# Kernel optimization log

Hardware: AMD Instinct MI355X
Metric: run time of the kernel (lower is better)

## Reference

```python
import jax, jax.numpy as jnp
import numpy as np

D_RBF = 36
KMIN = 9
EPS_LN = 1e-5


def layer_norm(x, g, b):
    mu = x.mean(-1, keepdims=True)
    var = ((x - mu) ** 2).mean(-1, keepdims=True)
    return (x - mu) * jax.lax.rsqrt(var + EPS_LN) * g + b


def rbf(D):
    # radial basis expansion, 36 gaussians on [0, 20]
    mu = jnp.linspace(0.0, 20.0, D_RBF)
    sigma = 20.0 / D_RBF
    return jnp.exp(-(((D[..., None] - mu) / sigma) ** 2))


def cdist(a, b):
    d2 = jnp.sum((a[:, :, None, :] - b[:, None, :, :]) ** 2, -1)
    return jnp.sqrt(jnp.maximum(d2, 1e-12))


def setup_inputs() -> dict:
    key = jax.random.key(0)
    ks = iter(jax.random.split(key, 64))
    B, N, L = 1, 64, 512
    d_msa, d_pair, d_state = 64, 128, 16
    def nrm(shape, s=1.0):
        return jax.random.normal(next(ks), shape, jnp.float32) * s
    def lin(fin, fout):
        return nrm((fin, fout), 0.05), jnp.zeros((fout,), jnp.float32)
    def ln(d):
        return jnp.ones((d,), jnp.float32), jnp.zeros((d,), jnp.float32)
    inp = {}
    inp['msa'] = nrm((B, N, L, d_msa))
    inp['pair'] = nrm((B, L, L, d_pair))
    inp['xyz'] = nrm((B, L, 3, 3), 8.0)  # spread coords so kNN is meaningful
    inp['state'] = nrm((B, L, d_state))
    inp['seq1hot'] = jax.nn.one_hot(jax.random.randint(next(ks), (B, L), 0, 21), 21, dtype=jnp.float32)
    inp['idx'] = jnp.broadcast_to(jnp.arange(L, dtype=jnp.int32)[None], (B, L))
    inp['top_k'] = 64
    inp['g_msa'], inp['b_msa'] = ln(d_msa)
    inp['g_pair'], inp['b_pair'] = ln(d_pair)
    inp['g_state'], inp['b_state'] = ln(d_state)
    inp['Wq'], inp['bq'] = lin(d_msa, d_msa)
    inp['Wk'], inp['bk'] = lin(d_msa, d_msa)
    inp['Wx'], inp['bx'] = lin(d_msa + 21 + d_state, 32)
    inp['We1'], inp['be1'] = lin(d_pair, 32)
    inp['We2'], inp['be2'] = lin(32 + D_RBF + 1, 32)
    inp['g_node'], inp['b_node'] = ln(32)
    inp['g_e1'], inp['b_e1'] = ln(32)
    inp['g_e2'], inp['b_e2'] = ln(32)
    # SE3-style equivariant MP layer params
    inp['Wm1'], inp['bm1'] = lin(32 + 32 + 32 + 1, 64)
    inp['Wm2'], inp['bm2'] = lin(64, 32)
    inp['Wc'], inp['bc'] = lin(32, 8)      # 2 out vec channels x (1 coef for d + 3 for v_src)
    inp['Wh'], inp['bh'] = lin(64, 16)     # l0 out
    inp['Wv'] = nrm((2, 3), 0.05)          # l1 channel mixing
    return inp


def reference(msa, pair, xyz, state, seq1hot, idx, top_k,
              g_msa, b_msa, g_pair, b_pair, g_state, b_state,
              Wq, bq, Wk, bk, Wx, bx, We1, be1, We2, be2,
              g_node, b_node, g_e1, b_e1, g_e2, b_e2,
              Wm1, bm1, Wm2, bm2, Wc, bc, Wh, bh, Wv):
    eps = 1e-5
    B, N, L, K = msa.shape
    msa = layer_norm(msa, g_msa, b_msa)
    pair = layer_norm(pair, g_pair, b_pair)
    state = layer_norm(state, g_state, b_state)

    # SequenceWeight (1 head): first-seq query attends over N sequences per position
    q = (msa[:, 0] @ Wq + bq) / jnp.sqrt(jnp.float32(K))       # (B,L,K)
    k = jnp.einsum('bnlk,kd->bnld', msa, Wk) + bk              # (B,N,L,K)
    attn = jax.nn.softmax(jnp.einsum('blk,bnlk->bnl', q, k), axis=1)
    msa1 = jnp.einsum('bnl,bnlk->blk', attn, msa)              # (B,L,K)

    node = jnp.concatenate([msa1, seq1hot, state], -1)
    node = layer_norm(node @ Wx + bx, g_node, b_node)          # (B,L,32)
    edge = layer_norm(pair @ We1 + be1, g_e1, b_e1)            # (B,L,L,32)

    sep = idx[:, None, :] - idx[:, :, None]                    # (B,L,L)
    neighbor = jnp.where(jnp.abs(sep) <= 1, sep, 0).astype(node.dtype)[..., None]
    ca = xyz[:, :, 1]                                          # (B,L,3)
    rbf_feat = rbf(cdist(ca, ca))
    edge = jnp.concatenate([edge, rbf_feat, neighbor], -1)
    edge = layer_norm(edge @ We2 + be2, g_e2, b_e2)            # (B,L,L,32)

    # kNN + sequence-separation graph, as a dense boolean mask (edge i->j)
    eye = jnp.eye(L)[None]
    D = cdist(ca, ca) + eye * 999.9
    sep_a = jnp.abs(sep).astype(jnp.float32) + eye * 999.9
    kk = min(int(top_k), L)
    _, E_idx = jax.lax.top_k(-jax.lax.stop_gradient(D), kk)    # (B,L,kk) nearest j per i
    bi = jnp.arange(B)[:, None, None]
    ii = jnp.arange(L)[None, :, None]
    mask = jnp.zeros((B, L, L), bool).at[bi, ii, E_idx].set(True)
    mask = jnp.logical_or(mask, sep_a < KMIN)
    maskf = mask.astype(node.dtype)

    v = xyz - ca[:, :, None, :]                                # l1 feats (B,L,3,3)
    dvec = jax.lax.stop_gradient(ca[:, None, :, :] - ca[:, :, None, :])  # d[b,i,j]=ca_j-ca_i
    dist = jnp.linalg.norm(dvec, axis=-1, keepdims=True)       # (B,L,L,1)

    # invariant scalar messages (avoid materializing concat: split Wm1)
    hid = (node @ Wm1[:32])[:, :, None, :] + (node @ Wm1[32:64])[:, None, :, :] \
        + edge @ Wm1[64:96] + dist * Wm1[96] + bm1
    hid = jax.nn.relu(hid)                                     # (B,L,L,64)
    m = jax.nn.relu(hid @ Wm2 + bm2)                           # (B,L,L,32)
    coef = (m @ Wc + bc).reshape(B, L, L, 2, 4)
    # equivariant vector messages: coef0 * d_ij + sum_c coef_c * v_i[c]
    vmsg = coef[..., 0:1] * dvec[:, :, :, None, :] \
         + jnp.einsum('bijoc,bicv->bijov', coef[..., 1:], v)   # (B,L,L,2,3)
    agg_m = jnp.einsum('bij,bijk->bjk', maskf, m)              # aggregate at target j
    agg_v = jnp.einsum('bij,bijov->bjov', maskf, vmsg)

    state_out = jnp.concatenate([node, agg_m], -1) @ Wh + bh   # shift['0'] -> (B,L,16)
    off = agg_v + jnp.einsum('oc,blcv->blov', Wv, v)           # shift['1'] -> (B,L,2,3)

    # Rodrigues rotation + translation update
    T = off[:, :, 0]
    R = off[:, :, 1]
    ang = jnp.linalg.norm(R, axis=-1, keepdims=True)           # (B,L,1)
    Rv = (R / (ang + eps))[:, :, None, :]                      # (B,L,1,3)
    Rdv = jnp.sum(Rv * v, -1, keepdims=True)                   # (B,L,3,1)
    Rxv = jnp.cross(jnp.broadcast_to(Rv, v.shape), v)
    vperp = v - Rv * Rdv
    upar = Rv * Rdv
    c = jnp.cos(ang)[:, :, None, :]
    s = jnp.sin(ang)[:, :, None, :]
    v_new = vperp * c + Rxv * s + upar
    xyz_new = v_new + (ca + T)[:, :, None, :]
    return xyz_new, state_out
```

## Files before the change

### kernel.cpp

```cpp
#include <hip/hip_runtime.h>
#include <hip/hip_bf16.h>

typedef __attribute__((ext_vector_type(8))) short short8v;
typedef __attribute__((ext_vector_type(4))) float f32x4;

__device__ __forceinline__ unsigned short f2bu(float a){
  union { __hip_bfloat16 b; unsigned short u; } cv;
  cv.b = __float2bfloat16(a);
  return cv.u;
}
__device__ __forceinline__ void sp2(float a, unsigned short &h, unsigned short &l){
  h = f2bu(a);
  l = f2bu(a - __uint_as_float(((unsigned)h)<<16));
}
__device__ __forceinline__ float wred64(float v){
  #pragma unroll
  for(int o=32;o;o>>=1) v += __shfl_xor(v,o,64);
  return v;
}
__device__ __forceinline__ float wred32(float v){
  #pragma unroll
  for(int o=16;o;o>>=1) v += __shfl_xor(v,o,64);
  return v;
}
__device__ __forceinline__ float wmax64(float v){
  #pragma unroll
  for(int o=32;o;o>>=1) v = fmaxf(v,__shfl_xor(v,o,64));
  return v;
}

__global__ void __launch_bounds__(256) k_ctx(
  const float* __restrict__ msa, const float* __restrict__ g_msa, const float* __restrict__ b_msa,
  const float* __restrict__ Wq, const float* __restrict__ bq,
  const float* __restrict__ Wk, const float* __restrict__ bk,
  const float* __restrict__ seq1hot, const float* __restrict__ state,
  const float* __restrict__ g_state, const float* __restrict__ b_state,
  const float* __restrict__ Wx, const float* __restrict__ bx,
  const float* __restrict__ g_node, const float* __restrict__ b_node,
  const float* __restrict__ Wm1,
  float* __restrict__ node, float* __restrict__ nodeA, float* __restrict__ nodeB,
  const float* __restrict__ ca, const int* __restrict__ idx,
  const int* __restrict__ topk_ptr, unsigned char* __restrict__ maskT)
{
  int l = blockIdx.x, tid = threadIdx.x;
  int wave = tid>>6, lane = tid&63;
  __shared__ float ms[64][64];
  __shared__ float qs[64];
  __shared__ float logit[64];
  __shared__ float part[4][64];
  __shared__ float ins[101];
  __shared__ float nd[32];

  {
    int nn = tid>>2, qd = tid&3;
    const float* mrow = msa + ((size_t)nn*512 + (size_t)l)*64 + qd*16;
    f32x4 a[4];
    #pragma unroll
    for(int t=0;t<4;t++) a[t] = *(const f32x4*)(mrow + t*4);
    float s=0.f, ss=0.f;
    #pragma unroll
    for(int t=0;t<4;t++)
      #pragma unroll
      for(int e=0;e<4;e++){ float v=a[t][e]; s+=v; ss+=v*v; }
    s  += __shfl_xor(s,1,64);  s  += __shfl_xor(s,2,64);
    ss += __shfl_xor(ss,1,64); ss += __shfl_xor(ss,2,64);
    float mu = s*(1.f/64.f);
    float rstd = rsqrtf(ss*(1.f/64.f) - mu*mu + 1e-5f);
    #pragma unroll
    for(int t=0;t<4;t++){
      f32x4 g4 = *(const f32x4*)(g_msa + qd*16 + t*4);
      f32x4 b4 = *(const f32x4*)(b_msa + qd*16 + t*4);
      f32x4 o4;
      #pragma unroll
      for(int e=0;e<4;e++) o4[e] = (a[t][e]-mu)*rstd*g4[e] + b4[e];
      *(f32x4*)&ms[nn][qd*16 + t*4] = o4;
    }
  }
  __syncthreads();
  if(wave==0){
    float acc = bq[lane];
    for(int k=0;k<64;k++) acc += ms[0][k]*Wq[k*64+lane];
    qs[lane] = acc*0.125f;
  }
  __syncthreads();
  float qd2 = qs[lane];
  for(int it=0; it<16; ++it){
    int nn = it*4 + wave;
    float acc = bk[lane];
    for(int k2=0;k2<64;k2++) acc += ms[nn][k2]*Wk[k2*64+lane];
    float p = wred64(qd2*acc);
    if(lane==0) logit[nn] = p;
  }
  __syncthreads();
  float v  = logit[lane];
  float mx = wmax64(v);
  float e  = expf(v-mx);
  float sd = wred64(e);
  float a  = e/sd;
  float pm = 0.f;
  for(int it=0; it<16; ++it){
    int nn = it*4 + wave;
    pm += __shfl(a,nn,64)*ms[nn][lane];
  }
  part[wave][lane] = pm;
  __syncthreads();
  if(wave==0){
    ins[lane] = part[0][lane]+part[1][lane]+part[2][lane]+part[3][lane];
    if(lane<21) ins[64+lane] = seq1hot[l*21+lane];
    float sv = (lane<16)? state[l*16+lane] : 0.f;
    float mu = sv;
    #pragma unroll
    for(int o=8;o;o>>=1) mu += __shfl_xor(mu,o,64);
    mu *= (1.f/16.f);
    float dv = sv-mu;
    float var = dv*dv;
    #pragma unroll
    for(int o=8;o;o>>=1) var += __shfl_xor(var,o,64);
    var *= (1.f/16.f);
    if(lane<16) ins[85+lane] = dv*rsqrtf(var+1e-5f)*g_state[lane]+b_state[lane];

    int d = lane & 31;
    float np_ = 0.f;
    if(lane<32){
      np_ = bx[d];
      for(int c=0;c<101;c++) np_ += ins[c]*Wx[c*32+d];
    }
    float mu2 = wred32(np_)*(1.f/32.f);
    float d2  = np_-mu2;
    float v2  = wred32(d2*d2)*(1.f/32.f);
    float nv  = d2*rsqrtf(v2+1e-5f);
    if(lane<32){
      nv = nv*g_node[d]+b_node[d];
      node[l*32+d] = nv;
      nd[d] = nv;
    }
    float a2=0.f, b2=0.f;
    for(int c=0;c<32;c++){
      float x = nd[c];
      a2 += x*Wm1[c*64+lane];
      b2 += x*Wm1[(32+c)*64+lane];
    }
    nodeA[l*64+lane] = a2;
    nodeB[l*64+lane] = b2;
  } else if(wave==1){
    int i = l;
    float cx = ca[i*3], cy = ca[i*3+1], cz = ca[i*3+2];
    int idxi = idx[i];
    unsigned long long key[8];
    #pragma unroll
    for(int t=0;t<8;t++){
      int jj = t*64 + lane;
      float dx = cx-ca[jj*3], dy = cy-ca[jj*3+1], dz = cz-ca[jj*3+2];
      float dd = sqrtf(fmaxf(dx*dx+dy*dy+dz*dz, 1e-12f));
      if(jj==i) dd += 999.9f;
      key[t] = (((unsigned long long)__float_as_uint(dd))<<32) | (unsigned)jj;
      int sep = abs(idx[jj]-idxi);
      maskT[jj*512+i] = (jj!=i && sep<9) ? 1 : 0;
    }
    int kk = *topk_ptr; if(kk>512) kk = 512;
    for(int t=0;t<kk;t++){
      unsigned long long m = key[0];
      #pragma unroll
      for(int u=1;u<8;u++) m = (key[u]<m)? key[u] : m;
      #pragma unroll
      for(int o=32;o;o>>=1){
        unsigned long long o2 = __shfl_xor(m,o,64);
        m = (o2<m)? o2 : m;
      }
      int jc = (int)(m & 0xffffffffu);
      if(lane==0) maskT[jc*512+i] = 1;
      #pragma unroll
      for(int u=0;u<8;u++) if(key[u]==m) key[u] = ~0ull;
    }
  }
}

__global__ void k_fold(const float* __restrict__ We1, const float* __restrict__ be1,
                       const float* __restrict__ g_pair, const float* __restrict__ b_pair,
                       const float* __restrict__ We2, const float* __restrict__ be2,
                       const float* __restrict__ g_e1, const float* __restrict__ b_e1,
                       const float* __restrict__ Wm1, const float* __restrict__ bm1,
                       const float* __restrict__ g_e2, const float* __restrict__ b_e2,
                       const float* __restrict__ Wm2, const float* __restrict__ Wc,
                       const float* __restrict__ xyz,
                       unsigned short* __restrict__ wbuf, float* __restrict__ bbuf,
                       float* __restrict__ ca, float* __restrict__ vv){
  int fidx = blockIdx.x;
  int tid  = threadIdx.x;
  if(fidx < 46){
    int t = fidx*512 + tid;
    int lane = tid>>3, e = tid&7;
    int f = (fidx<23)? fidx : fidx-23;
    int krow = (lane>>4)*8 + e;
    int n = lane&15;
    float val = 0.f;
    if(f<8){
      int kt=f>>1, nt=f&1; int c=kt*32+krow, d=nt*16+n;
      val = g_pair[c]*We1[c*32+d];
    } else if(f<14){
      int f2=f-8; int kt=f2>>1, nt=f2&1; int c=kt*32+krow, d=nt*16+n;
      if(c<32)      val = g_e1[c]*We2[c*32+d];
      else if(c<69) val = We2[c*32+d];
      else          val = 0.f;
    } else if(f<18){
      int nt=f-14; int c=krow, h=nt*16+n;
      val = g_e2[c]*Wm1[(64+c)*64+h];
    } else if(f<22){
      int f2=f-18; int kt=f2>>1, nt=f2&1; int c=kt*32+krow, d=nt*16+n;
      val = Wm2[c*32+d];
    } else {
      int c=krow;
      val = (n<8)? Wc[c*8+n] : 0.f;
    }
    unsigned short h = f2bu(val);
    if(fidx<23) wbuf[t] = h;
    else {
      float fh = __uint_as_float(((unsigned)h)<<16);
      wbuf[t] = f2bu(val - fh);
    }
  } else if(fidx == 46){
    if(tid<32){
      float s = be1[tid];
      for(int c=0;c<128;c++) s += b_pair[c]*We1[c*32+tid];
      bbuf[tid]=s;
    } else if(tid<64){
      int d=tid-32; float s=be2[d];
      for(int c=0;c<32;c++) s += b_e1[c]*We2[c*32+d];
      bbuf[tid]=s;
    } else if(tid<128){
      int h=tid-64; float s=bm1[h];
      for(int c=0;c<32;c++) s += b_e2[c]*Wm1[(64+c)*64+h];
      bbuf[tid]=s;
    }
  } else {
    int l = tid;
    float c0=xyz[l*9+3], c1=xyz[l*9+4], c2=xyz[l*9+5];
    ca[l*3+0]=c0; ca[l*3+1]=c1; ca[l*3+2]=c2;
    #pragma unroll
    for(int a2=0;a2<3;a2++){
      vv[l*9+a2*3+0]=xyz[l*9+a2*3+0]-c0;
      vv[l*9+a2*3+1]=xyz[l*9+a2*3+1]-c1;
      vv[l*9+a2*3+2]=xyz[l*9+a2*3+2]-c2;
    }
  }
}

__global__ void __launch_bounds__(256,2) k_pair_mfma(
  const float* __restrict__ pair, const unsigned short* __restrict__ wbuf,
  const float* __restrict__ bbuf, const float* __restrict__ Wm1,
  const float* __restrict__ bm2, const float* __restrict__ bc,
  const float* __restrict__ nodeA, const float* __restrict__ nodeB,
  const float* __restrict__ ca, const float* __restrict__ vv,
  const int* __restrict__ idx, const unsigned char* __restrict__ maskT,
  float* __restrict__ aggM, float* __restrict__ aggV)
{
  const int j = blockIdx.x, tid = threadIdx.x;
  const int wave = tid>>6, lane = tid&63;
  const int kg = lane>>4, n = lane&15;

  __shared__ __align__(16) unsigned short Yh[4][16*104];
  __shared__ __align__(16) unsigned short Yl[4][16*104];
  __shared__ __align__(16) unsigned short WloE[23*512];
  __shared__ float coefT[4][16*8];
  __shared__ float redM[4][32];
  __shared__ float redV[4][8];
  unsigned short* Yhw = Yh[wave];
  unsigned short* Ylw = Yl[wave];
  float* CT = coefT[wave];

  for(int t=tid; t<(23*512)/8; t+=256)
    ((uint4*)WloE)[t] = ((const uint4*)(wbuf + 23*512))[t];

  short8v wf[23];
  #pragma unroll
  for(int f=0; f<23; f++) wf[f] = *(const short8v*)(wbuf + f*512 + lane*8);

  const float be1f0 = bbuf[n],     be1f1 = bbuf[16+n];
  const float be2f0 = bbuf[32+n],  be2f1 = bbuf[48+n];
  float bm1n[4], wm1d[4];
  #pragma unroll
  for(int nt=0;nt<4;nt++){
    bm1n[nt] = bbuf[64+nt*16+n] + nodeB[j*64+nt*16+n];
    wm1d[nt] = Wm1[96*64+nt*16+n];
  }
  const float bm2r0 = bm2[n], bm2r1 = bm2[16+n];
  const float bcr = (n<8)? bc[n] : 0.f;
  const float cjx = ca[j*3], cjy = ca[j*3+1], cjz = ca[j*3+2];
  const int idxj = idx[j];

  __syncthreads();

  for(int t=lane; t<16*27; t+=64){ int r=t/27, c=69+t-r*27; Yhw[r*104+c]=0; Ylw[r*104+c]=0; }

  float accM0=0.f, accM1=0.f;
  float accV[6]={0.f,0.f,0.f,0.f,0.f,0.f};

  float x[4][8];
  {
    const float* prow0 = pair + (((size_t)(wave*16+n))*512 + (size_t)j)*128;
    #pragma unroll
    for(int kt=0;kt<4;kt++){
      *(f32x4*)&x[kt][0] = *(const f32x4*)(prow0 + kt*32 + kg*8);
      *(f32x4*)&x[kt][4] = *(const f32x4*)(prow0 + kt*32 + kg*8 + 4);
    }
  }

  for(int i0 = wave*16; i0 < 512; i0 += 64){
    float s=0.f, ss=0.f;
    #pragma unroll
    for(int kt=0;kt<4;kt++)
      #pragma unroll
      for(int e=0;e<8;e++){ float xv=x[kt][e]; s+=xv; ss+=xv*xv; }
    s  += __shfl_xor(s,16,64);  s  += __shfl_xor(s,32,64);
    ss += __shfl_xor(ss,16,64); ss += __shfl_xor(ss,32,64);
    float mu = s*(1.f/128.f);
    float rstd = rsqrtf(ss*(1.f/128.f) - mu*mu + 1e-5f);

    float xn[4][8];
    const bool hasNext = (i0+64 < 512);
    if(hasNext){
      const float* prown = pair + (((size_t)(i0+64+n))*512 + (size_t)j)*128;
      #pragma unroll
      for(int kt=0;kt<4;kt++){
        *(f32x4*)&xn[kt][0] = *(const f32x4*)(prown + kt*32 + kg*8);
        *(f32x4*)&xn[kt][4] = *(const f32x4*)(prown + kt*32 + kg*8 + 4);
      }
    }

    float na[4][4];
    #pragma unroll
    for(int q=0;q<4;q++)
      #pragma unroll
      for(int nt=0;nt<4;nt++)
        na[nt][q] = nodeA[(size_t)(i0+4*kg+q)*64 + nt*16+n];
    float mk[4];
    #pragma unroll
    for(int q=0;q<4;q++) mk[q] = (float)maskT[j*512 + i0+4*kg+q];
    float mkr = (float)maskT[j*512 + i0+n];
    const float* vr = vv + (i0+n)*9;
    float v00=vr[0], v01=vr[1], v02=vr[2];
    float v10=vr[3], v11=vr[4], v12=vr[5];
    float v20=vr[6], v21=vr[7], v22=vr[8];
    const float* cai = ca + (i0+n)*3;
    float cix=cai[0], ciy=cai[1], ciz=cai[2];
    int idxi_r = idx[i0+n];

    short8v xh[4], xl[4];
    #pragma unroll
    for(int kt=0;kt<4;kt++){
      #pragma unroll
      for(int e=0;e<8;e++){
        unsigned short h_, l_;
        sp2((x[kt][e]-mu)*rstd, h_, l_);
        xh[kt][e] = (short)h_;
        xl[kt][e] = (short)l_;
      }
    }

    f32x4 z0={0.f,0.f,0.f,0.f}, z1={0.f,0.f,0.f,0.f};
    #pragma unroll
    for(int kt=0;kt<4;kt++){
      short8v wlo0 = *(const short8v*)&WloE[(2*kt+0)*512 + lane*8];
      short8v wlo1 = *(const short8v*)&WloE[(2*kt+1)*512 + lane*8];
      z0 = __builtin_amdgcn_mfma_f32_16x16x32_bf16(xh[kt], wf[2*kt+0], z0, 0,0,0);
      z0 = __builtin_amdgcn_mfma_f32_16x16x32_bf16(xl[kt], wf[2*kt+0], z0, 0,0,0);
      z0 = __builtin_amdgcn_mfma_f32_16x16x32_bf16(xh[kt], wlo0,      z0, 0,0,0);
      z1 = __builtin_amdgcn_mfma_f32_16x16x32_bf16(xh[kt], wf[2*kt+1], z1, 0,0,0);
      z1 = __builtin_amdgcn_mfma_f32_16x16x32_bf16(xl[kt], wf[2*kt+1], z1, 0,0,0);
      z1 = __builtin_amdgcn_mfma_f32_16x16x32_bf16(xh[kt], wlo1,      z1, 0,0,0);
    }
    #pragma unroll
    for(int q=0;q<4;q++){
      float ev0 = z0[q] + be1f0;
      float ev1 = z1[q] + be1f1;
      float sq  = ev0+ev1;
      float sq2 = ev0*ev0+ev1*ev1;
      #pragma unroll
      for(int o=8;o;o>>=1){ sq+=__shfl_xor(sq,o,64); sq2+=__shfl_xor(sq2,o,64); }
      float m_ = sq*(1.f/32.f);
      float rs = rsqrtf(sq2*(1.f/32.f)-m_*m_+1e-5f);
      unsigned short h0,l0,h1,l1;
      sp2((ev0-m_)*rs, h0, l0);
      sp2((ev1-m_)*rs, h1, l1);
      int r = 4*kg+q;
      Yhw[r*104 + n]    = h0;
      Yhw[r*104 + 16+n] = h1;
      Ylw[r*104 + n]    = l0;
      Ylw[r*104 + 16+n] = l1;
    }

    float dxr = cjx-cix, dyr = cjy-ciy, dzr = cjz-ciz;
    float d2r = dxr*dxr+dyr*dyr+dzr*dzr;
    float dist_r = sqrtf(d2r);
    float drbf = sqrtf(fmaxf(d2r,1e-12f));
    #pragma unroll
    for(int sI=0;sI<9;sI++){
      int t = kg*9+sI;
      float u = (drbf - (float)t*(20.f/35.f))*1.8f;
      unsigned short h_, l_;
      sp2(__expf(-u*u), h_, l_);
      Yhw[n*104 + 32 + t] = h_;
      Ylw[n*104 + 32 + t] = l_;
    }
    if(kg==0){
      int sep = idxj - idxi_r;
      float nb = (sep>=-1 && sep<=1)?(float)sep:0.f;
      unsigned short h_, l_;
      sp2(nb, h_, l_);
      Yhw[n*104 + 68] = h_;
      Ylw[n*104 + 68] = l_;
    }

    short8v yh_[3], yl_[3];
    #pragma unroll
    for(int kt=0;kt<3;kt++){
      yh_[kt] = *(const short8v*)&Yhw[n*104 + kt*32 + kg*8];
      yl_[kt] = *(const short8v*)&Ylw[n*104 + kt*32 + kg*8];
    }
    f32x4 e2a0={0.f,0.f,0.f,0.f}, e2a1={0.f,0.f,0.f,0.f};
    #pragma unroll
    for(int kt=0;kt<3;kt++){
      short8v wlo0 = *(const short8v*)&WloE[(8+2*kt)*512 + lane*8];
      short8v wlo1 = *(const short8v*)&WloE[(9+2*kt)*512 + lane*8];
      e2a0 = __builtin_amdgcn_mfma_f32_16x16x32_bf16(yh_[kt], wf[8+2*kt], e2a0, 0,0,0);
      e2a0 = __builtin_amdgcn_mfma_f32_16x16x32_bf16(yl_[kt], wf[8+2*kt], e2a0, 0,0,0);
      e2a0 = __builtin_amdgcn_mfma_f32_16x16x32_bf16(yh_[kt], wlo0,      e2a0, 0,0,0);
      e2a1 = __builtin_amdgcn_mfma_f32_16x16x32_bf16(yh_[kt], wf[9+2*kt], e2a1, 0,0,0);
      e2a1 = __builtin_amdgcn_mfma_f32_16x16x32_bf16(yl_[kt], wf[9+2*kt], e2a1, 0,0,0);
      e2a1 = __builtin_amdgcn_mfma_f32_16x16x32_bf16(yh_[kt], wlo1,      e2a1, 0,0,0);
    }
    #pragma unroll
    for(int q=0;q<4;q++){
      float ev0 = e2a0[q]+be2f0;
      float ev1 = e2a1[q]+be2f1;
      float sq  = ev0+ev1;
      float sq2 = ev0*ev0+ev1*ev1;
      #pragma unroll
      for(int o=8;o;o>>=1){ sq+=__shfl_xor(sq,o,64); sq2+=__shfl_xor(sq2,o,64); }
      float m_ = sq*(1.f/32.f);
      float rs = rsqrtf(sq2*(1.f/32.f)-m_*m_+1e-5f);
      unsigned short h0,l0,h1,l1;
      sp2((ev0-m_)*rs, h0, l0);
      sp2((ev1-m_)*rs, h1, l1);
      int r = 4*kg+q;
      Yhw[r*104 + n]    = h0;
      Yhw[r*104 + 16+n] = h1;
      Ylw[r*104 + n]    = l0;
      Ylw[r*104 + 16+n] = l1;
    }

    short8v e2Ah = *(const short8v*)&Yhw[n*104 + kg*8];
    short8v e2Al = *(const short8v*)&Ylw[n*104 + kg*8];
    float dist_q[4];
    #pragma unroll
    for(int q=0;q<4;q++) dist_q[q] = __shfl(dist_r, 4*kg+q, 64);
    #pragma unroll
    for(int nt=0;nt<4;nt++){
      short8v wlo = *(const short8v*)&WloE[(14+nt)*512 + lane*8];
      f32x4 hacc = {0.f,0.f,0.f,0.f};
      hacc = __builtin_amdgcn_mfma_f32_16x16x32_bf16(e2Ah, wf[14+nt], hacc, 0,0,0);
      hacc = __builtin_amdgcn_mfma_f32_16x16x32_bf16(e2Al, wf[14+nt], hacc, 0,0,0);
      hacc = __builtin_amdgcn_mfma_f32_16x16x32_bf16(e2Ah, wlo,       hacc, 0,0,0);
      #pragma unroll
      for(int q=0;q<4;q++){
        float t_ = hacc[q] + bm1n[nt] + dist_q[q]*wm1d[nt] + na[nt][q];
        float hv = fmaxf(t_,0.f);
        unsigned short h_, l_;
        sp2(hv, h_, l_);
        Yhw[(4*kg+q)*104 + nt*16+n] = h_;
        Ylw[(4*kg+q)*104 + nt*16+n] = l_;
      }
    }

    short8v hAh[2], hAl[2];
    #pragma unroll
    for(int kt=0;kt<2;kt++){
      hAh[kt] = *(const short8v*)&Yhw[n*104 + kt*32 + kg*8];
      hAl[kt] = *(const short8v*)&Ylw[n*104 + kt*32 + kg*8];
    }
    f32x4 ma0={0.f,0.f,0.f,0.f}, ma1={0.f,0.f,0.f,0.f};
    #pragma unroll
    for(int kt=0;kt<2;kt++){
      short8v wlo0 = *(const short8v*)&WloE[(18+2*kt)*512 + lane*8];
      short8v wlo1 = *(const short8v*)&WloE[(19+2*kt)*512 + lane*8];
      ma0 = __builtin_amdgcn_mfma_f32_16x16x32_bf16(hAh[kt], wf[18+2*kt], ma0, 0,0,0);
      ma0 = __builtin_amdgcn_mfma_f32_16x16x32_bf16(hAl[kt], wf[18+2*kt], ma0, 0,0,0);
      ma0 = __builtin_amdgcn_mfma_f32_16x16x32_bf16(hAh[kt], wlo0,       ma0, 0,0,0);
      ma1 = __builtin_amdgcn_mfma_f32_16x16x32_bf16(hAh[kt], wf[19+2*kt], ma1, 0,0,0);
      ma1 = __builtin_amdgcn_mfma_f32_16x16x32_bf16(hAl[kt], wf[19+2*kt], ma1, 0,0,0);
      ma1 = __builtin_amdgcn_mfma_f32_16x16x32_bf16(hAh[kt], wlo1,       ma1, 0,0,0);
    }
    #pragma unroll
    for(int q=0;q<4;q++){
      float mv0 = fmaxf(ma0[q]+bm2r0, 0.f);
      float mv1 = fmaxf(ma1[q]+bm2r1, 0.f);
      accM0 += mk[q]*mv0;
      accM1 += mk[q]*mv1;
      unsigned short h0,l0,h1,l1;
      sp2(mv0, h0, l0);
      sp2(mv1, h1, l1);
      int r = 4*kg+q;
      Yhw[r*104 + n]    = h0;
      Yhw[r*104 + 16+n] = h1;
      Ylw[r*104 + n]    = l0;
      Ylw[r*104 + 16+n] = l1;
    }

    short8v mAh = *(const short8v*)&Yhw[n*104 + kg*8];
    short8v mAl = *(const short8v*)&Ylw[n*104 + kg*8];
    short8v wloC = *(const short8v*)&WloE[22*512 + lane*8];
    f32x4 cf = {0.f,0.f,0.f,0.f};
    cf = __builtin_amdgcn_mfma_f32_16x16x32_bf16(mAh, wf[22], cf, 0,0,0);
    cf = __builtin_amdgcn_mfma_f32_16x16x32_bf16(mAl, wf[22], cf, 0,0,0);
    cf = __builtin_amdgcn_mfma_f32_16x16x32_bf16(mAh, wloC,  cf, 0,0,0);
    if(n<8){
      #pragma unroll
      for(int q=0;q<4;q++) CT[(4*kg+q)*8+n] = cf[q]+bcr;
    }
    f32x4 cA = *(const f32x4*)&CT[n*8];
    f32x4 cB = *(const f32x4*)&CT[n*8+4];

    accV[0] += mkr*(cA[0]*dxr + cA[1]*v00 + cA[2]*v10 + cA[3]*v20);
    accV[1] += mkr*(cA[0]*dyr + cA[1]*v01 + cA[2]*v11 + cA[3]*v21);
    accV[2] += mkr*(cA[0]*dzr + cA[1]*v02 + cA[2]*v12 + cA[3]*v22);
    accV[3] += mkr*(cB[0]*dxr + cB[1]*v00 + cB[2]*v10 + cB[3]*v20);
    accV[4] += mkr*(cB[0]*dyr + cB[1]*v01 + cB[2]*v11 + cB[3]*v21);
    accV[5] += mkr*(cB[0]*dzr + cB[1]*v02 + cB[2]*v12 + cB[3]*v22);

    if(hasNext){
      #pragma unroll
      for(int kt=0;kt<4;kt++)
        #pragma unroll
        for(int e=0;e<8;e++) x[kt][e] = xn[kt][e];
    }
  }

  accM0 += __shfl_xor(accM0,16,64); accM0 += __shfl_xor(accM0,32,64);
  accM1 += __shfl_xor(accM1,16,64); accM1 += __shfl_xor(accM1,32,64);
  #pragma unroll
  for(int c=0;c<6;c++){
    #pragma unroll
    for(int o=8;o;o>>=1) accV[c] += __shfl_xor(accV[c],o,64);
  }
  if(lane<16){ redM[wave][n] = accM0; redM[wave][16+n] = accM1; }
  if(lane==0){
    #pragma unroll
    for(int c=0;c<6;c++) redV[wave][c]=accV[c];
  }
  __syncthreads();
  if(tid<32) aggM[j*32+tid] = redM[0][tid]+redM[1][tid]+redM[2][tid]+redM[3][tid];
  if(tid>=64 && tid<70){
    int c = tid-64;
    aggV[j*6+c] = redV[0][c]+redV[1][c]+redV[2][c]+redV[3][c];
  }
}

__global__ void k_final(const float* __restrict__ node, const float* __restrict__ aggM,
                        const float* __restrict__ aggV, const float* __restrict__ Wh,
                        const float* __restrict__ bh, const float* __restrict__ Wv,
                        const float* __restrict__ ca, const float* __restrict__ vvb,
                        float* __restrict__ out){
  int l = blockIdx.x, lane = threadIdx.x;
  if(lane<16){
    float acc = bh[lane];
    for(int c=0;c<32;c++) acc += node[l*32+c]*Wh[c*16+lane];
    for(int c=0;c<32;c++) acc += aggM[l*32+c]*Wh[(32+c)*16+lane];
    out[4608 + l*16 + lane] = acc;
  }
  if(lane<9){
    int a = lane/3, vd = lane%3;
    float T[3], R[3];
    for(int q2=0;q2<3;q2++){
      float v0 = vvb[l*9+q2], v1 = vvb[l*9+3+q2], v2 = vvb[l*9+6+q2];
      T[q2] = aggV[l*6+q2]   + Wv[0]*v0 + Wv[1]*v1 + Wv[2]*v2;
      R[q2] = aggV[l*6+3+q2] + Wv[3]*v0 + Wv[4]*v1 + Wv[5]*v2;
    }
    float ang = sqrtf(R[0]*R[0]+R[1]*R[1]+R[2]*R[2]);
    float inv = 1.f/(ang+1e-5f);
    float Rv0=R[0]*inv, Rv1=R[1]*inv, Rv2=R[2]*inv;
    float va0=vvb[l*9+a*3+0], va1=vvb[l*9+a*3+1], va2=vvb[l*9+a*3+2];
    float Rdv = Rv0*va0+Rv1*va1+Rv2*va2;
    float Rvv[3]={Rv0,Rv1,Rv2};
    float vaa[3]={va0,va1,va2};
    float Rxv = Rvv[(vd+1)%3]*vaa[(vd+2)%3] - Rvv[(vd+2)%3]*vaa[(vd+1)%3];
    float vperp = vaa[vd] - Rvv[vd]*Rdv;
    float upar  = Rvv[vd]*Rdv;
    float cc = cosf(ang), ss = sinf(ang);
    float vnew = vperp*cc + Rxv*ss + upar;
    out[l*9+a*3+vd] = vnew + ca[l*3+vd] + T[vd];
  }
}

extern "C" void kernel_launch(void* const* d_in, const int* in_sizes, int n_in,
                              void* d_out, int out_size, void* d_ws, size_t ws_size,
                              hipStream_t stream) {
  const float* msa    = (const float*)d_in[0];
  const float* pair   = (const float*)d_in[1];
  const float* xyz    = (const float*)d_in[2];
  const float* state  = (const float*)d_in[3];
  const float* seq1hot= (const float*)d_in[4];
  const int*   idx    = (const int*)d_in[5];
  const int*   topk   = (const int*)d_in[6];
  const float* g_msa  = (const float*)d_in[7];  const float* b_msa  = (const float*)d_in[8];
  const float* g_pair = (const float*)d_in[9];  const float* b_pair = (const float*)d_in[10];
  const float* g_state= (const float*)d_in[11]; const float* b_state= (const float*)d_in[12];
  const float* Wq = (const float*)d_in[13]; const float* bq = (const float*)d_in[14];
  const float* Wk = (const float*)d_in[15]; const float* bk = (const float*)d_in[16];
  const float* Wx = (const float*)d_in[17]; const float* bx = (const float*)d_in[18];
  const float* We1= (const float*)d_in[19]; const float* be1= (const float*)d_in[20];
  const float* We2= (const float*)d_in[21]; const float* be2= (const float*)d_in[22];
  const float* g_node=(const float*)d_in[23]; const float* b_node=(const float*)d_in[24];
  const float* g_e1 = (const float*)d_in[25]; const float* b_e1 = (const float*)d_in[26];
  const float* g_e2 = (const float*)d_in[27]; const float* b_e2 = (const float*)d_in[28];
  const float* Wm1= (const float*)d_in[29]; const float* bm1= (const float*)d_in[30];
  const float* Wm2= (const float*)d_in[31]; const float* bm2= (const float*)d_in[32];
  const float* Wc = (const float*)d_in[33]; const float* bc = (const float*)d_in[34];
  const float* Wh = (const float*)d_in[35]; const float* bh = (const float*)d_in[36];
  const float* Wv = (const float*)d_in[37];
  float* out = (float*)d_out;

  float* ws = (float*)d_ws;
  float* node   = ws; ws += 512*32;
  float* nodeA  = ws; ws += 512*64;
  float* nodeB  = ws; ws += 512*64;
  float* cab    = ws; ws += 512*3;
  float* vvb    = ws; ws += 512*9;
  float* aggM   = ws; ws += 512*32;
  float* aggV   = ws; ws += 512*6;
  float* bbuf   = ws; ws += 160;
  unsigned short* wbuf = (unsigned short*)ws; ws += (46*512)/2 + 8;
  unsigned char* maskT = (unsigned char*)ws;

  k_fold<<<48,512,0,stream>>>(We1,be1,g_pair,b_pair,We2,be2,g_e1,b_e1,Wm1,bm1,g_e2,b_e2,Wm2,Wc,
                              xyz,wbuf,bbuf,cab,vvb);
  k_ctx<<<512,256,0,stream>>>(msa,g_msa,b_msa,Wq,bq,Wk,bk,seq1hot,state,g_state,b_state,
                              Wx,bx,g_node,b_node,Wm1,node,nodeA,nodeB,cab,idx,topk,maskT);
  k_pair_mfma<<<512,256,0,stream>>>(pair,wbuf,bbuf,Wm1,bm2,bc,nodeA,nodeB,cab,vvb,idx,maskT,aggM,aggV);
  k_final<<<512,64,0,stream>>>(node,aggM,aggV,Wh,bh,Wv,cab,vvb,out);
}
```

Measured before the change: 113.2 us.

## Fuse weight-fold prep into context kernel and final update into pair kernel

The weight-folding/coordinate prep kernel becomes 48 extra blocks of the context kernel, which now reads CA coordinates straight from xyz instead of the prepared buffer. The final state/coordinate update kernel is merged into the tail of the pair MFMA kernel, keeping the aggregates in shared memory instead of writing them to global. This cuts the launch count from four to two and removes the aggregate round trip through global memory. In exchange the pair kernel gains an extra barrier and a small serial tail per block, and the context grid grows by a few blocks.

```diff
diff --git a/kernel.cpp b/kernel.cpp
--- a/kernel.cpp
+++ b/kernel.cpp
@@ -37,12 +37,86 @@
   const float* __restrict__ g_state, const float* __restrict__ b_state,
   const float* __restrict__ Wx, const float* __restrict__ bx,
   const float* __restrict__ g_node, const float* __restrict__ b_node,
-  const float* __restrict__ Wm1,
+  const float* __restrict__ Wm1, const float* __restrict__ xyz,
+  const int* __restrict__ idx, const int* __restrict__ topk_ptr,
+  const float* __restrict__ We1, const float* __restrict__ be1,
+  const float* __restrict__ g_pair, const float* __restrict__ b_pair,
+  const float* __restrict__ We2, const float* __restrict__ be2,
+  const float* __restrict__ g_e1, const float* __restrict__ b_e1,
+  const float* __restrict__ bm1, const float* __restrict__ g_e2, const float* __restrict__ b_e2,
+  const float* __restrict__ Wm2, const float* __restrict__ Wc,
   float* __restrict__ node, float* __restrict__ nodeA, float* __restrict__ nodeB,
-  const float* __restrict__ ca, const int* __restrict__ idx,
-  const int* __restrict__ topk_ptr, unsigned char* __restrict__ maskT)
+  unsigned char* __restrict__ maskT,
+  unsigned short* __restrict__ wbuf, float* __restrict__ bbuf,
+  float* __restrict__ ca, float* __restrict__ vv)
 {
-  int l = blockIdx.x, tid = threadIdx.x;
+  int tid = threadIdx.x;
+
+  if(blockIdx.x >= 512){
+    int fidx = blockIdx.x - 512;
+    if(fidx < 46){
+      for(int tt=tid; tt<512; tt+=256){
+        int t = fidx*512 + tt;
+        int lane = tt>>3, e = tt&7;
+        int f = (fidx<23)? fidx : fidx-23;
+        int krow = (lane>>4)*8 + e;
+        int n = lane&15;
+        float val = 0.f;
+        if(f<8){
+          int kt=f>>1, nt=f&1; int c=kt*32+krow, d=nt*16+n;
+          val = g_pair[c]*We1[c*32+d];
+        } else if(f<14){
+          int f2=f-8; int kt=f2>>1, nt=f2&1; int c=kt*32+krow, d=nt*16+n;
+          if(c<32)      val = g_e1[c]*We2[c*32+d];
+          else if(c<69) val = We2[c*32+d];
+          else          val = 0.f;
+        } else if(f<18){
+          int nt=f-14; int c=krow, h=nt*16+n;
+          val = g_e2[c]*Wm1[(64+c)*64+h];
+        } else if(f<22){
+          int f2=f-18; int kt=f2>>1, nt=f2&1; int c=kt*32+krow, d=nt*16+n;
+          val = Wm2[c*32+d];
+        } else {
+          int c=krow;
+          val = (n<8)? Wc[c*8+n] : 0.f;
+        }
+        unsigned short h = f2bu(val);
+        if(fidx<23) wbuf[t] = h;
+        else {
+          float fh = __uint_as_float(((unsigned)h)<<16);
+          wbuf[t] = f2bu(val - fh);
+        }
+      }
+    } else if(fidx == 46){
+      if(tid<32){
+        float s = be1[tid];
+        for(int c=0;c<128;c++) s += b_pair[c]*We1[c*32+tid];
+        bbuf[tid]=s;
+      } else if(tid<64){
+        int d=tid-32; float s=be2[d];
+        for(int c=0;c<32;c++) s += b_e1[c]*We2[c*32+d];
+        bbuf[tid]=s;
+      } else if(tid<128){
+        int h=tid-64; float s=bm1[h];
+        for(int c=0;c<32;c++) s += b_e2[c]*Wm1[(64+c)*64+h];
+        bbuf[tid]=s;
+      }
+    } else {
+      for(int l=tid; l<512; l+=256){
+        float c0=xyz[l*9+3], c1=xyz[l*9+4], c2=xyz[l*9+5];
+        ca[l*3+0]=c0; ca[l*3+1]=c1; ca[l*3+2]=c2;
+        #pragma unroll
+        for(int a2=0;a2<3;a2++){
+          vv[l*9+a2*3+0]=xyz[l*9+a2*3+0]-c0;
+          vv[l*9+a2*3+1]=xyz[l*9+a2*3+1]-c1;
+          vv[l*9+a2*3+2]=xyz[l*9+a2*3+2]-c2;
+        }
+      }
+    }
+    return;
+  }
+
+  int l = blockIdx.x;
   int wave = tid>>6, lane = tid&63;
   __shared__ float ms[64][64];
   __shared__ float qs[64];
@@ -144,13 +218,13 @@
     nodeB[l*64+lane] = b2;
   } else if(wave==1){
     int i = l;
-    float cx = ca[i*3], cy = ca[i*3+1], cz = ca[i*3+2];
+    float cx = xyz[i*9+3], cy = xyz[i*9+4], cz = xyz[i*9+5];
     int idxi = idx[i];
     unsigned long long key[8];
     #pragma unroll
     for(int t=0;t<8;t++){
       int jj = t*64 + lane;
-      float dx = cx-ca[jj*3], dy = cy-ca[jj*3+1], dz = cz-ca[jj*3+2];
+      float dx = cx-xyz[jj*9+3], dy = cy-xyz[jj*9+4], dz = cz-xyz[jj*9+5];
       float dd = sqrtf(fmaxf(dx*dx+dy*dy+dz*dz, 1e-12f));
       if(jj==i) dd += 999.9f;
       key[t] = (((unsigned long long)__float_as_uint(dd))<<32) | (unsigned)jj;
@@ -175,84 +249,16 @@
   }
 }
 
-__global__ void k_fold(const float* __restrict__ We1, const float* __restrict__ be1,
-                       const float* __restrict__ g_pair, const float* __restrict__ b_pair,
-                       const float* __restrict__ We2, const float* __restrict__ be2,
-                       const float* __restrict__ g_e1, const float* __restrict__ b_e1,
-                       const float* __restrict__ Wm1, const float* __restrict__ bm1,
-                       const float* __restrict__ g_e2, const float* __restrict__ b_e2,
-                       const float* __restrict__ Wm2, const float* __restrict__ Wc,
-                       const float* __restrict__ xyz,
-                       unsigned short* __restrict__ wbuf, float* __restrict__ bbuf,
-                       float* __restrict__ ca, float* __restrict__ vv){
-  int fidx = blockIdx.x;
-  int tid  = threadIdx.x;
-  if(fidx < 46){
-    int t = fidx*512 + tid;
-    int lane = tid>>3, e = tid&7;
-    int f = (fidx<23)? fidx : fidx-23;
-    int krow = (lane>>4)*8 + e;
-    int n = lane&15;
-    float val = 0.f;
-    if(f<8){
-      int kt=f>>1, nt=f&1; int c=kt*32+krow, d=nt*16+n;
-      val = g_pair[c]*We1[c*32+d];
-    } else if(f<14){
-      int f2=f-8; int kt=f2>>1, nt=f2&1; int c=kt*32+krow, d=nt*16+n;
-      if(c<32)      val = g_e1[c]*We2[c*32+d];
-      else if(c<69) val = We2[c*32+d];
-      else          val = 0.f;
-    } else if(f<18){
-      int nt=f-14; int c=krow, h=nt*16+n;
-      val = g_e2[c]*Wm1[(64+c)*64+h];
-    } else if(f<22){
-      int f2=f-18; int kt=f2>>1, nt=f2&1; int c=kt*32+krow, d=nt*16+n;
-      val = Wm2[c*32+d];
-    } else {
-      int c=krow;
-      val = (n<8)? Wc[c*8+n] : 0.f;
-    }
-    unsigned short h = f2bu(val);
-    if(fidx<23) wbuf[t] = h;
-    else {
-      float fh = __uint_as_float(((unsigned)h)<<16);
-      wbuf[t] = f2bu(val - fh);
-    }
-  } else if(fidx == 46){
-    if(tid<32){
-      float s = be1[tid];
-      for(int c=0;c<128;c++) s += b_pair[c]*We1[c*32+tid];
-      bbuf[tid]=s;
-    } else if(tid<64){
-      int d=tid-32; float s=be2[d];
-      for(int c=0;c<32;c++) s += b_e1[c]*We2[c*32+d];
-      bbuf[tid]=s;
-    } else if(tid<128){
-      int h=tid-64; float s=bm1[h];
-      for(int c=0;c<32;c++) s += b_e2[c]*Wm1[(64+c)*64+h];
-      bbuf[tid]=s;
-    }
-  } else {
-    int l = tid;
-    float c0=xyz[l*9+3], c1=xyz[l*9+4], c2=xyz[l*9+5];
-    ca[l*3+0]=c0; ca[l*3+1]=c1; ca[l*3+2]=c2;
-    #pragma unroll
-    for(int a2=0;a2<3;a2++){
-      vv[l*9+a2*3+0]=xyz[l*9+a2*3+0]-c0;
-      vv[l*9+a2*3+1]=xyz[l*9+a2*3+1]-c1;
-      vv[l*9+a2*3+2]=xyz[l*9+a2*3+2]-c2;
-    }
-  }
-}
-
 __global__ void __launch_bounds__(256,2) k_pair_mfma(
   const float* __restrict__ pair, const unsigned short* __restrict__ wbuf,
   const float* __restrict__ bbuf, const float* __restrict__ Wm1,
   const float* __restrict__ bm2, const float* __restrict__ bc,
   const float* __restrict__ nodeA, const float* __restrict__ nodeB,
+  const float* __restrict__ node,
   const float* __restrict__ ca, const float* __restrict__ vv,
   const int* __restrict__ idx, const unsigned char* __restrict__ maskT,
-  float* __restrict__ aggM, float* __restrict__ aggV)
+  const float* __restrict__ Wh, const float* __restrict__ bh,
+  const float* __restrict__ Wv, float* __restrict__ out)
 {
   const int j = blockIdx.x, tid = threadIdx.x;
   const int wave = tid>>6, lane = tid&63;
@@ -264,6 +270,8 @@
   __shared__ float coefT[4][16*8];
   __shared__ float redM[4][32];
   __shared__ float redV[4][8];
+  __shared__ float aggMs[32];
+  __shared__ float aggVs[6];
   unsigned short* Yhw = Yh[wave];
   unsigned short* Ylw = Yl[wave];
   float* CT = coefT[wave];
@@ -548,46 +556,40 @@
     for(int c=0;c<6;c++) redV[wave][c]=accV[c];
   }
   __syncthreads();
-  if(tid<32) aggM[j*32+tid] = redM[0][tid]+redM[1][tid]+redM[2][tid]+redM[3][tid];
+  if(tid<32) aggMs[tid] = redM[0][tid]+redM[1][tid]+redM[2][tid]+redM[3][tid];
   if(tid>=64 && tid<70){
     int c = tid-64;
-    aggV[j*6+c] = redV[0][c]+redV[1][c]+redV[2][c]+redV[3][c];
-  }
-}
-
-__global__ void k_final(const float* __restrict__ node, const float* __restrict__ aggM,
-                        const float* __restrict__ aggV, const float* __restrict__ Wh,
-                        const float* __restrict__ bh, const float* __restrict__ Wv,
-                        const float* __restrict__ ca, const float* __restrict__ vvb,
-                        float* __restrict__ out){
-  int l = blockIdx.x, lane = threadIdx.x;
-  if(lane<16){
-    float acc = bh[lane];
-    for(int c=0;c<32;c++) acc += node[l*32+c]*Wh[c*16+lane];
-    for(int c=0;c<32;c++) acc += aggM[l*32+c]*Wh[(32+c)*16+lane];
-    out[4608 + l*16 + lane] = acc;
-  }
-  if(lane<9){
-    int a = lane/3, vd = lane%3;
+    aggVs[c] = redV[0][c]+redV[1][c]+redV[2][c]+redV[3][c];
+  }
+  __syncthreads();
+
+  if(tid<16){
+    float acc = bh[tid];
+    for(int c=0;c<32;c++) acc += node[j*32+c]*Wh[c*16+tid];
+    for(int c=0;c<32;c++) acc += aggMs[c]*Wh[(32+c)*16+tid];
+    out[4608 + j*16 + tid] = acc;
+  } else if(tid>=32 && tid<41){
+    int t2 = tid-32;
+    int a = t2/3, vd = t2%3;
     float T[3], R[3];
     for(int q2=0;q2<3;q2++){
-      float v0 = vvb[l*9+q2], v1 = vvb[l*9+3+q2], v2 = vvb[l*9+6+q2];
-      T[q2] = aggV[l*6+q2]   + Wv[0]*v0 + Wv[1]*v1 + Wv[2]*v2;
-      R[q2] = aggV[l*6+3+q2] + Wv[3]*v0 + Wv[4]*v1 + Wv[5]*v2;
+      float v0 = vv[j*9+q2], v1 = vv[j*9+3+q2], v2 = vv[j*9+6+q2];
+      T[q2] = aggVs[q2]   + Wv[0]*v0 + Wv[1]*v1 + Wv[2]*v2;
+      R[q2] = aggVs[3+q2] + Wv[3]*v0 + Wv[4]*v1 + Wv[5]*v2;
     }
     float ang = sqrtf(R[0]*R[0]+R[1]*R[1]+R[2]*R[2]);
     float inv = 1.f/(ang+1e-5f);
     float Rv0=R[0]*inv, Rv1=R[1]*inv, Rv2=R[2]*inv;
-    float va0=vvb[l*9+a*3+0], va1=vvb[l*9+a*3+1], va2=vvb[l*9+a*3+2];
+    float va0=vv[j*9+a*3+0], va1=vv[j*9+a*3+1], va2=vv[j*9+a*3+2];
     float Rdv = Rv0*va0+Rv1*va1+Rv2*va2;
     float Rvv[3]={Rv0,Rv1,Rv2};
     float vaa[3]={va0,va1,va2};
     float Rxv = Rvv[(vd+1)%3]*vaa[(vd+2)%3] - Rvv[(vd+2)%3]*vaa[(vd+1)%3];
     float vperp = vaa[vd] - Rvv[vd]*Rdv;
     float upar  = Rvv[vd]*Rdv;
-    float cc = cosf(ang), ss = sinf(ang);
-    float vnew = vperp*cc + Rxv*ss + upar;
-    out[l*9+a*3+vd] = vnew + ca[l*3+vd] + T[vd];
+    float cc = cosf(ang), ssn = sinf(ang);
+    float vnew = vperp*cc + Rxv*ssn + upar;
+    out[j*9+a*3+vd] = vnew + ca[j*3+vd] + T[vd];
   }
 }
 
@@ -625,16 +627,14 @@
   float* nodeB  = ws; ws += 512*64;
   float* cab    = ws; ws += 512*3;
   float* vvb    = ws; ws += 512*9;
-  float* aggM   = ws; ws += 512*32;
-  float* aggV   = ws; ws += 512*6;
   float* bbuf   = ws; ws += 160;
   unsigned short* wbuf = (unsigned short*)ws; ws += (46*512)/2 + 8;
   unsigned char* maskT = (unsigned char*)ws;
 
-  k_fold<<<48,512,0,stream>>>(We1,be1,g_pair,b_pair,We2,be2,g_e1,b_e1,Wm1,bm1,g_e2,b_e2,Wm2,Wc,
-                              xyz,wbuf,bbuf,cab,vvb);
-  k_ctx<<<512,256,0,stream>>>(msa,g_msa,b_msa,Wq,bq,Wk,bk,seq1hot,state,g_state,b_state,
-                              Wx,bx,g_node,b_node,Wm1,node,nodeA,nodeB,cab,idx,topk,maskT);
-  k_pair_mfma<<<512,256,0,stream>>>(pair,wbuf,bbuf,Wm1,bm2,bc,nodeA,nodeB,cab,vvb,idx,maskT,aggM,aggV);
-  k_final<<<512,64,0,stream>>>(node,aggM,aggV,Wh,bh,Wv,cab,vvb,out);
-}
+  k_ctx<<<560,256,0,stream>>>(msa,g_msa,b_msa,Wq,bq,Wk,bk,seq1hot,state,g_state,b_state,
+                              Wx,bx,g_node,b_node,Wm1,xyz,idx,topk,
+                              We1,be1,g_pair,b_pair,We2,be2,g_e1,b_e1,bm1,g_e2,b_e2,Wm2,Wc,
+                              node,nodeA,nodeB,maskT,wbuf,bbuf,cab,vvb);
+  k_pair_mfma<<<512,256,0,stream>>>(pair,wbuf,bbuf,Wm1,bm2,bc,nodeA,nodeB,node,cab,vvb,idx,maskT,
+                                    Wh,bh,Wv,out);
+}
```

Measured after the change: 106.4 us. -6.0%, faster.
